# Optimization experiments

Hardware: AMD Instinct MI355X
Metric: run time of the kernel (lower is better)

## Reference

```python
import jax, jax.numpy as jnp
import numpy as np

B, C, N = 4, 192, 4096
K = 16                      # avg degree
E = B * N * K               # 262144 edges
C_OUT = 384


def setup_inputs() -> dict:
    key = jax.random.key(0)
    k1, k2, k3, k4 = jax.random.split(key, 4)
    x = jax.random.normal(k1, (B, C, N, 1), dtype=jnp.float32)
    edge_index = jax.random.randint(k2, (2, E), 0, B * N, dtype=jnp.int64)
    # BasicConv([2C, C_OUT]): 1x1 Conv2d + bias + ReLU (norm=None)
    W = jax.random.normal(k3, (C_OUT, 2 * C), dtype=jnp.float32) * (1.0 / np.sqrt(2 * C))
    b = jax.random.normal(k4, (C_OUT,), dtype=jnp.float32) * 0.01
    return {"x": x, "edge_index": edge_index, "W": W, "b": b}


def reference(x, edge_index, W, b):
    Bs, Cs, Ns, _ = x.shape
    BN = Bs * Ns
    # (B,C,N,1) -> flattened node table (B*N, C); node id = b*N + n
    x_flat = jnp.transpose(x[..., 0], (0, 2, 1)).reshape(BN, Cs)
    x_i = x_flat[edge_index[0]]          # (E, C) gather at dst
    x_j = x_flat[edge_index[1]]          # (E, C) gather at src
    diff = x_j - x_i
    # scatter-max over dst nodes; torch_scatter fills empty segments with 0
    agg = jax.ops.segment_max(diff, edge_index[0], num_segments=BN)
    agg = jnp.where(jnp.isfinite(agg), agg, 0.0)
    x_j_out = jnp.transpose(agg.reshape(Bs, Ns, Cs), (0, 2, 1))[..., None]  # (B,C,N,1)
    # interleave channels: cat along new axis 2 then reshape -> (B, 2C, N, 1)
    cat = jnp.stack([x, x_j_out], axis=2).reshape(Bs, 2 * Cs, Ns, 1)
    # 1x1 conv == GEMM over channels, + bias + ReLU
    out = jnp.einsum('oc,bcnw->bonw', W, cat) + b[None, :, None, None]
    return jax.nn.relu(out)
```

## Files before the change

kernel.cpp:

```cpp
#include <hip/hip_runtime.h>
#include <hip/hip_bf16.h>
#include <math.h>

#define Bz    4
#define Cch   192
#define Nn    4096
#define BN    16384
#define Ecnt  262144
#define COUT  384
#define CAP   64

typedef __attribute__((ext_vector_type(8))) short short8;
typedef __attribute__((ext_vector_type(4))) float floatx4;

__device__ __forceinline__ void gload_lds16(const void* g, void* l) {
    __builtin_amdgcn_global_load_lds(
        (const __attribute__((address_space(1))) unsigned int*)g,
        (__attribute__((address_space(3))) unsigned int*)l, 16, 0, 0);
}

__global__ void detect_kernel(const unsigned int* __restrict__ ew, int* __restrict__ flag) {
    __shared__ int s;
    if (threadIdx.x == 0) s = 1;
    __syncthreads();
    if (ew[2 * threadIdx.x + 1] != 0u) atomicAnd(&s, 0);
    __syncthreads();
    if (threadIdx.x == 0) *flag = s;
}

__device__ __forceinline__ int edge_at(const int* __restrict__ ew, int is64, int elem) {
    return is64 ? ew[2 * elem] : ew[elem];
}

__global__ void transpose_kernel(const float* __restrict__ x, __hip_bfloat16* __restrict__ xb) {
    __shared__ float tile[32][33];
    int b  = blockIdx.z;
    int c0 = blockIdx.y * 32;
    int n0 = blockIdx.x * 32;
    for (int i = threadIdx.y; i < 32; i += 8)
        tile[i][threadIdx.x] = x[((size_t)(b * Cch + c0 + i)) * Nn + n0 + threadIdx.x];
    __syncthreads();
    for (int i = threadIdx.y; i < 32; i += 8)
        xb[((size_t)(b * Nn + n0 + i)) * Cch + c0 + threadIdx.x] =
            __float2bfloat16(tile[threadIdx.x][i]);
}

__global__ void convw_kernel(const float* __restrict__ W,
                             __hip_bfloat16* __restrict__ Wx, __hip_bfloat16* __restrict__ Wa) {
    int i = blockIdx.x * 256 + threadIdx.x;
    if (i >= COUT * Cch) return;
    int o = i / Cch, c = i - o * Cch;
    Wx[i] = __float2bfloat16(W[o * 2 * Cch + 2 * c]);
    Wa[i] = __float2bfloat16(W[o * 2 * Cch + 2 * c + 1]);
}

__global__ void fill_kernel(const int* __restrict__ ew, const int* __restrict__ flag,
                            int* __restrict__ deg, int* __restrict__ slots) {
    int e = blockIdx.x * blockDim.x + threadIdx.x;
    if (e >= Ecnt) return;
    int is64 = *flag;
    int dst = edge_at(ew, is64, e);
    int src = edge_at(ew, is64, Ecnt + e);
    int p = atomicAdd(&deg[dst], 1);
    if (p < CAP) slots[(dst << 6) + p] = src;
}

__global__ void agg_kernel(const int* __restrict__ deg, const int* __restrict__ slots,
                           const __hip_bfloat16* __restrict__ xb,
                           __hip_bfloat16* __restrict__ aggb) {
    int node = blockIdx.x;
    int c = threadIdx.x;
    __shared__ int nbr[CAP];
    int d = deg[node]; if (d > CAP) d = CAP;
    if (c < d) nbr[c] = slots[(node << 6) + c];
    __syncthreads();
    float m = -INFINITY;
    int k = 0;
    for (; k + 4 <= d; k += 4) {
        int s0 = nbr[k], s1 = nbr[k + 1], s2 = nbr[k + 2], s3 = nbr[k + 3];
        float v0 = __bfloat162float(xb[s0 * Cch + c]);
        float v1 = __bfloat162float(xb[s1 * Cch + c]);
        float v2 = __bfloat162float(xb[s2 * Cch + c]);
        float v3 = __bfloat162float(xb[s3 * Cch + c]);
        m = fmaxf(m, fmaxf(fmaxf(v0, v1), fmaxf(v2, v3)));
    }
    for (; k < d; k++) m = fmaxf(m, __bfloat162float(xb[nbr[k] * Cch + c]));
    float xv = __bfloat162float(xb[node * Cch + c]);
    float r = (d > 0) ? (m - xv) : 0.0f;
    aggb[node * Cch + c] = __float2bfloat16(r);
}

__global__ __launch_bounds__(256) void gemm_kernel(
    const __hip_bfloat16* __restrict__ Xb, const __hip_bfloat16* __restrict__ Ab,
    const __hip_bfloat16* __restrict__ Wx, const __hip_bfloat16* __restrict__ Wa,
    const float* __restrict__ bias, float* __restrict__ out) {
    __shared__ short As[64 * 32];
    __shared__ short Bs[64 * 32];
    int t = threadIdx.x;
    int node0 = blockIdx.x * 64;
    int o0    = blockIdx.y * 64;
    int lane = t & 63, wave = t >> 6;
    int quad = lane >> 4, lrow = lane & 15;
    int wm = wave & 1, wn = wave >> 1;

    floatx4 acc[2][2] = {};
    int srow = t >> 2;
    int koff = (t & 3) * 8;

    const __hip_bfloat16* Asrc[2] = {Xb, Ab};
    const __hip_bfloat16* Bsrc[2] = {Wx, Wa};

    for (int seg = 0; seg < 2; seg++) {
        const __hip_bfloat16* a_g = Asrc[seg] + (size_t)(node0 + srow) * Cch + koff;
        const __hip_bfloat16* b_g = Bsrc[seg] + (size_t)(o0 + srow) * Cch + koff;
        for (int kt = 0; kt < Cch; kt += 32) {
            __syncthreads();
            gload_lds16(a_g + kt, &As[t * 8]);
            gload_lds16(b_g + kt, &Bs[t * 8]);
            __syncthreads();
            short8 af0 = *(const short8*)&As[(wm * 32 + lrow) * 32 + quad * 8];
            short8 af1 = *(const short8*)&As[(wm * 32 + 16 + lrow) * 32 + quad * 8];
            short8 bf0 = *(const short8*)&Bs[(wn * 32 + lrow) * 32 + quad * 8];
            short8 bf1 = *(const short8*)&Bs[(wn * 32 + 16 + lrow) * 32 + quad * 8];
            acc[0][0] = __builtin_amdgcn_mfma_f32_16x16x32_bf16(bf0, af0, acc[0][0], 0, 0, 0);
            acc[1][0] = __builtin_amdgcn_mfma_f32_16x16x32_bf16(bf0, af1, acc[1][0], 0, 0, 0);
            acc[0][1] = __builtin_amdgcn_mfma_f32_16x16x32_bf16(bf1, af0, acc[0][1], 0, 0, 0);
            acc[1][1] = __builtin_amdgcn_mfma_f32_16x16x32_bf16(bf1, af1, acc[1][1], 0, 0, 0);
        }
    }

#pragma unroll
    for (int im = 0; im < 2; im++) {
        int node = node0 + wm * 32 + im * 16 + lrow;
        int b = node >> 12, n = node & 4095;
#pragma unroll
        for (int in = 0; in < 2; in++) {
            int ob = o0 + wn * 32 + in * 16 + quad * 4;
#pragma unroll
            for (int r = 0; r < 4; r++) {
                int o = ob + r;
                float v = acc[im][in][r] + bias[o];
                out[((size_t)(b * COUT + o)) * Nn + n] = fmaxf(v, 0.0f);
            }
        }
    }
}

extern "C" void kernel_launch(void* const* d_in, const int* in_sizes, int n_in,
                              void* d_out, int out_size, void* d_ws, size_t ws_size,
                              hipStream_t stream) {
    const float* x    = (const float*)d_in[0];
    const int*   ew   = (const int*)d_in[1];
    const float* W    = (const float*)d_in[2];
    const float* bias = (const float*)d_in[3];
    float* out        = (float*)d_out;

    char* ws = (char*)d_ws;
    __hip_bfloat16* xb   = (__hip_bfloat16*)ws;
    __hip_bfloat16* aggb = (__hip_bfloat16*)(ws + 6291456);
    __hip_bfloat16* Wx   = (__hip_bfloat16*)(ws + 12582912);
    __hip_bfloat16* Wa   = (__hip_bfloat16*)(ws + 12730368);
    int* deg   = (int*)(ws + 12877824);
    int* slots = (int*)(ws + 12943360);
    int* flag  = (int*)(ws + 17137664);

    hipMemsetAsync(deg, 0, BN * sizeof(int), stream);
    detect_kernel<<<1, 256, 0, stream>>>((const unsigned int*)ew, flag);
    convw_kernel<<<(COUT * Cch + 255) / 256, 256, 0, stream>>>(W, Wx, Wa);
    transpose_kernel<<<dim3(Nn / 32, Cch / 32, Bz), dim3(32, 8), 0, stream>>>(x, xb);
    fill_kernel<<<Ecnt / 256, 256, 0, stream>>>(ew, flag, deg, slots);
    agg_kernel<<<BN, Cch, 0, stream>>>(deg, slots, xb, aggb);
    gemm_kernel<<<dim3(BN / 64, COUT / 64), 256, 0, stream>>>(xb, aggb, Wx, Wa, bias, out);
}
```

Baseline: 131.5 us.

## Fuse prep kernels, vectorize edge fill, and use wave-per-node aggregation

Merges the memset, dtype-detect, weight conversion and transpose into one block-partitioned prep kernel, which cuts launch count and per-launch overhead. The fill kernel now handles two edges per thread with vector loads. The aggregation kernel assigns one wavefront per node, passes neighbor indices with shuffles instead of LDS plus a barrier, and loads 4 bf16 channels per lane. In exchange, 16 of the 64 lanes sit idle in aggregation, and the fused prep kernel has heterogeneous blocks.

```diff
diff --git a/kernel.cpp b/kernel.cpp
--- a/kernel.cpp
+++ b/kernel.cpp
@@ -19,75 +19,114 @@
         (__attribute__((address_space(3))) unsigned int*)l, 16, 0, 0);
 }
 
-__global__ void detect_kernel(const unsigned int* __restrict__ ew, int* __restrict__ flag) {
-    __shared__ int s;
-    if (threadIdx.x == 0) s = 1;
-    __syncthreads();
-    if (ew[2 * threadIdx.x + 1] != 0u) atomicAnd(&s, 0);
-    __syncthreads();
-    if (threadIdx.x == 0) *flag = s;
-}
-
-__device__ __forceinline__ int edge_at(const int* __restrict__ ew, int is64, int elem) {
-    return is64 ? ew[2 * elem] : ew[elem];
-}
-
-__global__ void transpose_kernel(const float* __restrict__ x, __hip_bfloat16* __restrict__ xb) {
-    __shared__ float tile[32][33];
-    int b  = blockIdx.z;
-    int c0 = blockIdx.y * 32;
-    int n0 = blockIdx.x * 32;
-    for (int i = threadIdx.y; i < 32; i += 8)
-        tile[i][threadIdx.x] = x[((size_t)(b * Cch + c0 + i)) * Nn + n0 + threadIdx.x];
-    __syncthreads();
-    for (int i = threadIdx.y; i < 32; i += 8)
-        xb[((size_t)(b * Nn + n0 + i)) * Cch + c0 + threadIdx.x] =
-            __float2bfloat16(tile[threadIdx.x][i]);
-}
-
-__global__ void convw_kernel(const float* __restrict__ W,
-                             __hip_bfloat16* __restrict__ Wx, __hip_bfloat16* __restrict__ Wa) {
-    int i = blockIdx.x * 256 + threadIdx.x;
-    if (i >= COUT * Cch) return;
-    int o = i / Cch, c = i - o * Cch;
-    Wx[i] = __float2bfloat16(W[o * 2 * Cch + 2 * c]);
-    Wa[i] = __float2bfloat16(W[o * 2 * Cch + 2 * c + 1]);
-}
-
-__global__ void fill_kernel(const int* __restrict__ ew, const int* __restrict__ flag,
-                            int* __restrict__ deg, int* __restrict__ slots) {
-    int e = blockIdx.x * blockDim.x + threadIdx.x;
-    if (e >= Ecnt) return;
-    int is64 = *flag;
-    int dst = edge_at(ew, is64, e);
-    int src = edge_at(ew, is64, Ecnt + e);
-    int p = atomicAdd(&deg[dst], 1);
-    if (p < CAP) slots[(dst << 6) + p] = src;
-}
-
-__global__ void agg_kernel(const int* __restrict__ deg, const int* __restrict__ slots,
-                           const __hip_bfloat16* __restrict__ xb,
-                           __hip_bfloat16* __restrict__ aggb) {
-    int node = blockIdx.x;
-    int c = threadIdx.x;
-    __shared__ int nbr[CAP];
+__device__ __forceinline__ float b2f(unsigned short u) {
+    union { unsigned int i; float f; } z; z.i = ((unsigned int)u) << 16; return z.f;
+}
+__device__ __forceinline__ unsigned short f2b(float f) {
+    __hip_bfloat16 h = __float2bfloat16(f);
+    return *(unsigned short*)&h;
+}
+
+__global__ __launch_bounds__(256) void prep_kernel(
+    const float* __restrict__ x, const unsigned int* __restrict__ ew,
+    const float* __restrict__ W, __hip_bfloat16* __restrict__ xb,
+    __hip_bfloat16* __restrict__ Wx, __hip_bfloat16* __restrict__ Wa,
+    int* __restrict__ deg, int* __restrict__ flag) {
+    int bid = blockIdx.x;
+    if (bid < 3072) {
+        __shared__ float tile[32][33];
+        int b = bid / 768;
+        int r = bid - b * 768;
+        int c0 = (r >> 7) * 32;
+        int n0 = (r & 127) * 32;
+        int tx = threadIdx.x & 31, ty = threadIdx.x >> 5;
+        for (int i = ty; i < 32; i += 8)
+            tile[i][tx] = x[((size_t)(b * Cch + c0 + i)) * Nn + n0 + tx];
+        __syncthreads();
+        for (int i = ty; i < 32; i += 8)
+            xb[((size_t)(b * Nn + n0 + i)) * Cch + c0 + tx] =
+                __float2bfloat16(tile[tx][i]);
+    } else if (bid < 3360) {
+        int i = (bid - 3072) * 256 + threadIdx.x;
+        int o = i / Cch, c = i - o * Cch;
+        Wx[i] = __float2bfloat16(W[o * 2 * Cch + 2 * c]);
+        Wa[i] = __float2bfloat16(W[o * 2 * Cch + 2 * c + 1]);
+    } else if (bid < 3424) {
+        deg[(bid - 3360) * 256 + threadIdx.x] = 0;
+    } else {
+        __shared__ int s;
+        if (threadIdx.x == 0) s = 1;
+        __syncthreads();
+        if (ew[2 * threadIdx.x + 1] != 0u) atomicAnd(&s, 0);
+        __syncthreads();
+        if (threadIdx.x == 0) *flag = s;
+    }
+}
+
+__global__ __launch_bounds__(256) void fill_kernel(
+    const int* __restrict__ ew, const int* __restrict__ flag,
+    int* __restrict__ deg, int* __restrict__ slots) {
+    int t = blockIdx.x * 256 + threadIdx.x;
+    int d0, d1, s0, s1;
+    if (*flag) {
+        int4 dv = *(const int4*)&ew[4 * t];
+        int4 sv = *(const int4*)&ew[2 * Ecnt + 4 * t];
+        d0 = dv.x; d1 = dv.z; s0 = sv.x; s1 = sv.z;
+    } else {
+        int2 dv = *(const int2*)&ew[2 * t];
+        int2 sv = *(const int2*)&ew[Ecnt + 2 * t];
+        d0 = dv.x; d1 = dv.y; s0 = sv.x; s1 = sv.y;
+    }
+    int p0 = atomicAdd(&deg[d0], 1); if (p0 < CAP) slots[(d0 << 6) + p0] = s0;
+    int p1 = atomicAdd(&deg[d1], 1); if (p1 < CAP) slots[(d1 << 6) + p1] = s1;
+}
+
+__global__ __launch_bounds__(256) void agg_kernel(
+    const int* __restrict__ deg, const int* __restrict__ slots,
+    const __hip_bfloat16* __restrict__ xb, __hip_bfloat16* __restrict__ aggb) {
+    int lane = threadIdx.x & 63, wave = threadIdx.x >> 6;
+    int node = (blockIdx.x << 2) + wave;
     int d = deg[node]; if (d > CAP) d = CAP;
-    if (c < d) nbr[c] = slots[(node << 6) + c];
-    __syncthreads();
-    float m = -INFINITY;
+    int nbrval = 0;
+    if (lane < d) nbrval = slots[(node << 6) + lane];
+    const unsigned short* xbu = (const unsigned short*)xb;
+    int act = lane < 48;
+    int cb = lane * 4;
+    float m0 = -INFINITY, m1 = -INFINITY, m2 = -INFINITY, m3 = -INFINITY;
     int k = 0;
     for (; k + 4 <= d; k += 4) {
-        int s0 = nbr[k], s1 = nbr[k + 1], s2 = nbr[k + 2], s3 = nbr[k + 3];
-        float v0 = __bfloat162float(xb[s0 * Cch + c]);
-        float v1 = __bfloat162float(xb[s1 * Cch + c]);
-        float v2 = __bfloat162float(xb[s2 * Cch + c]);
-        float v3 = __bfloat162float(xb[s3 * Cch + c]);
-        m = fmaxf(m, fmaxf(fmaxf(v0, v1), fmaxf(v2, v3)));
-    }
-    for (; k < d; k++) m = fmaxf(m, __bfloat162float(xb[nbr[k] * Cch + c]));
-    float xv = __bfloat162float(xb[node * Cch + c]);
-    float r = (d > 0) ? (m - xv) : 0.0f;
-    aggb[node * Cch + c] = __float2bfloat16(r);
+        int s0 = __shfl(nbrval, k);
+        int s1 = __shfl(nbrval, k + 1);
+        int s2 = __shfl(nbrval, k + 2);
+        int s3 = __shfl(nbrval, k + 3);
+        if (act) {
+            ushort4 v0 = *(const ushort4*)&xbu[s0 * Cch + cb];
+            ushort4 v1 = *(const ushort4*)&xbu[s1 * Cch + cb];
+            ushort4 v2 = *(const ushort4*)&xbu[s2 * Cch + cb];
+            ushort4 v3 = *(const ushort4*)&xbu[s3 * Cch + cb];
+            m0 = fmaxf(fmaxf(m0, b2f(v0.x)), fmaxf(fmaxf(b2f(v1.x), b2f(v2.x)), b2f(v3.x)));
+            m1 = fmaxf(fmaxf(m1, b2f(v0.y)), fmaxf(fmaxf(b2f(v1.y), b2f(v2.y)), b2f(v3.y)));
+            m2 = fmaxf(fmaxf(m2, b2f(v0.z)), fmaxf(fmaxf(b2f(v1.z), b2f(v2.z)), b2f(v3.z)));
+            m3 = fmaxf(fmaxf(m3, b2f(v0.w)), fmaxf(fmaxf(b2f(v1.w), b2f(v2.w)), b2f(v3.w)));
+        }
+    }
+    for (; k < d; k++) {
+        int s = __shfl(nbrval, k);
+        if (act) {
+            ushort4 v = *(const ushort4*)&xbu[s * Cch + cb];
+            m0 = fmaxf(m0, b2f(v.x)); m1 = fmaxf(m1, b2f(v.y));
+            m2 = fmaxf(m2, b2f(v.z)); m3 = fmaxf(m3, b2f(v.w));
+        }
+    }
+    if (act) {
+        ushort4 xv = *(const ushort4*)&xbu[node * Cch + cb];
+        ushort4 o4;
+        o4.x = (d > 0) ? f2b(m0 - b2f(xv.x)) : 0;
+        o4.y = (d > 0) ? f2b(m1 - b2f(xv.y)) : 0;
+        o4.z = (d > 0) ? f2b(m2 - b2f(xv.z)) : 0;
+        o4.w = (d > 0) ? f2b(m3 - b2f(xv.w)) : 0;
+        *(ushort4*)&((unsigned short*)aggb)[node * Cch + cb] = o4;
+    }
 }
 
 __global__ __launch_bounds__(256) void gemm_kernel(
@@ -164,11 +203,8 @@
     int* slots = (int*)(ws + 12943360);
     int* flag  = (int*)(ws + 17137664);
 
-    hipMemsetAsync(deg, 0, BN * sizeof(int), stream);
-    detect_kernel<<<1, 256, 0, stream>>>((const unsigned int*)ew, flag);
-    convw_kernel<<<(COUT * Cch + 255) / 256, 256, 0, stream>>>(W, Wx, Wa);
-    transpose_kernel<<<dim3(Nn / 32, Cch / 32, Bz), dim3(32, 8), 0, stream>>>(x, xb);
-    fill_kernel<<<Ecnt / 256, 256, 0, stream>>>(ew, flag, deg, slots);
-    agg_kernel<<<BN, Cch, 0, stream>>>(deg, slots, xb, aggb);
+    prep_kernel<<<3425, 256, 0, stream>>>(x, (const unsigned int*)ew, W, xb, Wx, Wa, deg, flag);
+    fill_kernel<<<Ecnt / 512, 256, 0, stream>>>(ew, flag, deg, slots);
+    agg_kernel<<<BN / 4, 256, 0, stream>>>(deg, slots, xb, aggb);
     gemm_kernel<<<dim3(BN / 64, COUT / 64), 256, 0, stream>>>(xb, aggb, Wx, Wa, bias, out);
 }
```

After: 115.8 us. 12.0% less time.
